# Kernel tuning notes

Measured on AMD Instinct MI355X. Metric: run time of the kernel, lower is better.

## Reference

```python
import jax, jax.numpy as jnp
import numpy as np

B, N, O, C, K = 2, 384, 4, 128, 64  # batch, num_points, num_ori, num_hidden, basis_dim

def setup_inputs() -> dict:
    key = jax.random.key(0)
    ks = jax.random.split(key, 5)
    return {
        "x": jax.random.normal(ks[0], (B, N, O, C), dtype=jnp.float32),
        "kernel_basis": jax.random.normal(ks[1], (B, N, N, O, K), dtype=jnp.float32),
        "fiber_kernel_basis": jax.random.normal(ks[2], (O, O, K), dtype=jnp.float32),
        "W_spatial": jax.random.normal(ks[3], (K, C), dtype=jnp.float32) / np.sqrt(K),
        "W_rot": jax.random.normal(ks[4], (K, C), dtype=jnp.float32) / np.sqrt(K),
        "bias": jnp.zeros((C,), dtype=jnp.float32),
    }

def reference(x, kernel_basis, fiber_kernel_basis, W_spatial, W_rot, bias):
    # Dense projections (no bias), as in nn.Dense(num_hidden, use_bias=False)
    spatial_kernel = jnp.einsum('bmnok,kc->bmnoc', kernel_basis, W_spatial)   # (B,M,N,O,C)
    rot_kernel = jnp.einsum('pok,kc->poc', fiber_kernel_basis, W_rot)         # (O,O,C)
    # Spatial aggregation over source points n
    y = jnp.einsum('bnoc,bmnoc->bmoc', x, spatial_kernel)                     # (B,M,O,C)
    # Fiber (orientation) aggregation over o
    y = jnp.einsum('bmoc,poc->bmpc', y, rot_kernel)                           # (B,M,O,C)
    return y + bias
```

## Files before the change

kernel.cpp:

```cpp
#include <hip/hip_runtime.h>
#include <hip/hip_bf16.h>

typedef __attribute__((ext_vector_type(4)))  float    f32x4;
typedef __attribute__((ext_vector_type(16))) float    f32x16;
typedef __attribute__((ext_vector_type(8)))  _Float16 f16x8;

#define NB 2
#define NN 384
#define NO 4
#define NC 128
#define NK 64
#define MT 64
#define NMT 6
#define LDA 72
#define LDZ 72

__global__ __launch_bounds__(256, 3)
void sepconv_stage1(const float* __restrict__ KB, const float* __restrict__ X,
                    const float* __restrict__ Ws, float* __restrict__ part,
                    int ns)
{
    __shared__ _Float16 Alds[MT * LDA];
    __shared__ _Float16 Zlds[NC * LDZ];

    const int t  = threadIdx.x;
    const int wg = blockIdx.x;
    const int b  = wg & 1;
    const int o  = (wg >> 1) & 3;
    const int mt = (wg >> 3) % NMT;
    const int split = wg / (8 * NMT);
    const int n0 = split * ns;

    const int zc = t >> 1;
    const int kh = t & 1;
    float wreg[32];
#pragma unroll
    for (int j = 0; j < 32; ++j)
        wreg[j] = Ws[(kh * 32 + j) * NC + zc];

    const int ar  = t >> 2;
    const int ak0 = (t & 3) * 16;
    const int m   = mt * MT + ar;
    const int abase = (b * NN + m) * (NN * NO * NK) + o * NK + ak0;
    const int xbase = (b * NN) * (NO * NC) + o * NC + zc;

    const int lane = t & 63;
    const int wv   = t >> 6;
    const int msub = wv & 1;
    const int cs0  = wv >> 1;
    const int cs1  = 2 + (wv >> 1);
    const int half = lane >> 5;
    const int l31  = lane & 31;
    const _Float16* afp  = &Alds[(msub * 32 + l31) * LDA + half * 8];
    const _Float16* bfp0 = &Zlds[(cs0  * 32 + l31) * LDZ + half * 8];
    const _Float16* bfp1 = &Zlds[(cs1  * 32 + l31) * LDZ + half * 8];

    f32x16 acc0, acc1;
#pragma unroll
    for (int r = 0; r < 16; ++r) { acc0[r] = 0.f; acc1[r] = 0.f; }

    f32x4 acur[4];
    float xcur;
    {
        const float* ap = KB + abase + n0 * (NO * NK);
#pragma unroll
        for (int j = 0; j < 4; ++j) acur[j] = ((const f32x4*)ap)[j];
        xcur = X[xbase + n0 * (NO * NC)];
    }

    for (int i = 0; i < ns; ++i) {
        const int np = n0 + ((i + 1 < ns) ? (i + 1) : i);
        f32x4 anext[4];
        {
            const float* ap = KB + abase + np * (NO * NK);
#pragma unroll
            for (int j = 0; j < 4; ++j) anext[j] = ((const f32x4*)ap)[j];
        }
        const float xnext = X[xbase + np * (NO * NC)];

#pragma unroll
        for (int v = 0; v < 4; ++v) {
            f16x8 z;
#pragma unroll
            for (int j = 0; j < 8; ++j) z[j] = (_Float16)(xcur * wreg[v * 8 + j]);
            *(f16x8*)&Zlds[zc * LDZ + kh * 32 + v * 8] = z;
        }
#pragma unroll
        for (int v = 0; v < 2; ++v) {
            f16x8 a;
#pragma unroll
            for (int j = 0; j < 8; ++j)
                a[j] = (_Float16)(acur[v * 2 + (j >> 2)][j & 3]);
            *(f16x8*)&Alds[ar * LDA + ak0 + v * 8] = a;
        }
        __syncthreads();

#pragma unroll
        for (int kc = 0; kc < 4; ++kc) {
            f16x8 af  = *(const f16x8*)(afp  + kc * 16);
            f16x8 bf0 = *(const f16x8*)(bfp0 + kc * 16);
            f16x8 bf1 = *(const f16x8*)(bfp1 + kc * 16);
            acc0 = __builtin_amdgcn_mfma_f32_32x32x16_f16(af, bf0, acc0, 0, 0, 0);
            acc1 = __builtin_amdgcn_mfma_f32_32x32x16_f16(af, bf1, acc1, 0, 0, 0);
        }
        __syncthreads();

#pragma unroll
        for (int j = 0; j < 4; ++j) acur[j] = anext[j];
        xcur = xnext;
    }

    float* pb = part + ((size_t)((split * NB + b) * NO + o)) * (NN * NC);
#pragma unroll
    for (int r = 0; r < 16; ++r) {
        const int ml = (r & 3) + 8 * (r >> 2) + 4 * half;
        const int mm = mt * MT + msub * 32 + ml;
        pb[mm * NC + cs0 * 32 + l31] = acc0[r];
        pb[mm * NC + cs1 * 32 + l31] = acc1[r];
    }
}

__global__ __launch_bounds__(256)
void sepconv_stage2(const float* __restrict__ part, const float* __restrict__ fiber,
                    const float* __restrict__ Wr, const float* __restrict__ bias,
                    float* __restrict__ out, int nsplit)
{
    const int bid = blockIdx.x;
    const int b = bid / NN;
    const int m = bid % NN;
    const int t = threadIdx.x;
    const int c = t & 127;
    const int g = t >> 7;

    float rot[8];
#pragma unroll
    for (int i = 0; i < 8; ++i) rot[i] = 0.f;
    for (int k = 0; k < NK; ++k) {
        const float w = Wr[k * NC + c];
#pragma unroll
        for (int q = 0; q < 2; ++q)
#pragma unroll
            for (int oo = 0; oo < 4; ++oo)
                rot[q * 4 + oo] += fiber[((2 * g + q) * NO + oo) * NK + k] * w;
    }

    float y1[4];
#pragma unroll
    for (int oo = 0; oo < 4; ++oo) {
        float s = 0.f;
        for (int sp = 0; sp < nsplit; ++sp)
            s += part[((size_t)((sp * NB + b) * NO + oo)) * (NN * NC) + m * NC + c];
        y1[oo] = s;
    }

    const float bv = bias[c];
#pragma unroll
    for (int q = 0; q < 2; ++q) {
        float v = bv;
#pragma unroll
        for (int oo = 0; oo < 4; ++oo) v += y1[oo] * rot[q * 4 + oo];
        out[((b * NN + m) * NO + (2 * g + q)) * NC + c] = v;
    }
}

extern "C" void kernel_launch(void* const* d_in, const int* in_sizes, int n_in,
                              void* d_out, int out_size, void* d_ws, size_t ws_size,
                              hipStream_t stream)
{
    const float* X    = (const float*)d_in[0];
    const float* KB   = (const float*)d_in[1];
    const float* FB   = (const float*)d_in[2];
    const float* Ws   = (const float*)d_in[3];
    const float* Wr   = (const float*)d_in[4];
    const float* bias = (const float*)d_in[5];
    float* out  = (float*)d_out;
    float* part = (float*)d_ws;

    const size_t per = (size_t)NB * NO * NN * NC * sizeof(float);
    int nsplit = 16;
    while (nsplit > 1 && (size_t)nsplit * per > ws_size) nsplit >>= 1;
    const int ns = NN / nsplit;

    sepconv_stage1<<<dim3(8 * NMT * nsplit), dim3(256), 0, stream>>>(KB, X, Ws, part, ns);
    sepconv_stage2<<<dim3(NB * NN), dim3(256), 0, stream>>>(part, FB, Wr, bias, out, nsplit);
}
```

Before: 457.8 us.

## Stream kernel-basis tiles into LDS asynchronously and build B operand in registers

After: 491.7 us. +7.4%, slower.

```diff
diff --git a/kernel.cpp b/kernel.cpp
--- a/kernel.cpp
+++ b/kernel.cpp
@@ -1,5 +1,4 @@
 #include <hip/hip_runtime.h>
-#include <hip/hip_bf16.h>
 
 typedef __attribute__((ext_vector_type(4)))  float    f32x4;
 typedef __attribute__((ext_vector_type(16))) float    f32x16;
@@ -10,114 +9,122 @@
 #define NO 4
 #define NC 128
 #define NK 64
-#define MT 64
-#define NMT 6
-#define LDA 72
-#define LDZ 72
+#define MT 128
+#define NMT 3
 
-__global__ __launch_bounds__(256, 3)
+__device__ __forceinline__ void async16(const float* g, float* l) {
+    __builtin_amdgcn_global_load_lds((const __attribute__((address_space(1))) void*)g,
+                                     (__attribute__((address_space(3))) void*)l, 16, 0, 0);
+}
+
+__global__ __launch_bounds__(256, 2)
 void sepconv_stage1(const float* __restrict__ KB, const float* __restrict__ X,
                     const float* __restrict__ Ws, float* __restrict__ part,
                     int ns)
 {
-    __shared__ _Float16 Alds[MT * LDA];
-    __shared__ _Float16 Zlds[NC * LDZ];
+    extern __shared__ float smem[];
+    float* Abuf = smem;
+    float* xlds = smem + 4 * 2 * 2048;
 
-    const int t  = threadIdx.x;
-    const int wg = blockIdx.x;
-    const int b  = wg & 1;
-    const int o  = (wg >> 1) & 3;
-    const int mt = (wg >> 3) % NMT;
-    const int split = wg / (8 * NMT);
-    const int n0 = split * ns;
+    const int t    = threadIdx.x;
+    const int lane = t & 63;
+    const int w    = t >> 6;
+    const int l31  = lane & 31;
+    const int half = lane >> 5;
 
-    const int zc = t >> 1;
-    const int kh = t & 1;
-    float wreg[32];
+    const int wg    = blockIdx.x;
+    const int b     = wg & 1;
+    const int o     = (wg >> 1) & 3;
+    const int mt    = (wg >> 3) % NMT;
+    const int split = wg / 24;
+    const int n0    = split * ns;
+
+    f16x8 wsreg[4][4];
+    {
+        const float* wp = Ws + half * 8 * NC + l31;
 #pragma unroll
-    for (int j = 0; j < 32; ++j)
-        wreg[j] = Ws[(kh * 32 + j) * NC + zc];
-
-    const int ar  = t >> 2;
-    const int ak0 = (t & 3) * 16;
-    const int m   = mt * MT + ar;
-    const int abase = (b * NN + m) * (NN * NO * NK) + o * NK + ak0;
-    const int xbase = (b * NN) * (NO * NC) + o * NC + zc;
-
-    const int lane = t & 63;
-    const int wv   = t >> 6;
-    const int msub = wv & 1;
-    const int cs0  = wv >> 1;
-    const int cs1  = 2 + (wv >> 1);
-    const int half = lane >> 5;
-    const int l31  = lane & 31;
-    const _Float16* afp  = &Alds[(msub * 32 + l31) * LDA + half * 8];
-    const _Float16* bfp0 = &Zlds[(cs0  * 32 + l31) * LDZ + half * 8];
-    const _Float16* bfp1 = &Zlds[(cs1  * 32 + l31) * LDZ + half * 8];
-
-    f32x16 acc0, acc1;
+        for (int cs = 0; cs < 4; ++cs)
 #pragma unroll
-    for (int r = 0; r < 16; ++r) { acc0[r] = 0.f; acc1[r] = 0.f; }
-
-    f32x4 acur[4];
-    float xcur;
-    {
-        const float* ap = KB + abase + n0 * (NO * NK);
+            for (int kc = 0; kc < 4; ++kc) {
+                f16x8 v;
 #pragma unroll
-        for (int j = 0; j < 4; ++j) acur[j] = ((const f32x4*)ap)[j];
-        xcur = X[xbase + n0 * (NO * NC)];
+                for (int j = 0; j < 8; ++j)
+                    v[j] = (_Float16)wp[(kc * 16 + j) * NC + cs * 32];
+                wsreg[cs][kc] = v;
+            }
     }
 
+    for (int idx = t; idx < ns * NC; idx += 256) {
+        const int nl = idx >> 7, c = idx & 127;
+        xlds[idx] = X[((b * NN + n0 + nl) * NO + o) * NC + c];
+    }
+    __syncthreads();
+
+    const int mrow = mt * MT + w * 32 + l31;
+    const float* gbase = KB + (size_t)(b * NN + mrow) * (NN * NO * NK)
+                            + (size_t)n0 * (NO * NK) + o * NK + half * 4;
+    float* const wbuf = Abuf + w * 2 * 2048;
+
+    auto stage = [&](int nl, int p) {
+        const float* g = gbase + (size_t)nl * (NO * NK);
+        float* l = wbuf + p * 2048;
+#pragma unroll
+        for (int i = 0; i < 8; ++i)
+            async16(g + i * 8, l + i * 256);
+    };
+
+    f32x16 acc[4];
+#pragma unroll
+    for (int cs = 0; cs < 4; ++cs)
+#pragma unroll
+        for (int r = 0; r < 16; ++r) acc[cs][r] = 0.f;
+
+    stage(0, 0);
+    stage(1, 1);
+
     for (int i = 0; i < ns; ++i) {
-        const int np = n0 + ((i + 1 < ns) ? (i + 1) : i);
-        f32x4 anext[4];
-        {
-            const float* ap = KB + abase + np * (NO * NK);
+        if (i < ns - 1) __builtin_amdgcn_s_waitcnt(0x0F78);
+        else            __builtin_amdgcn_s_waitcnt(0x0F70);
+        __builtin_amdgcn_sched_barrier(0);
+
+        f16x8 xh[4];
 #pragma unroll
-            for (int j = 0; j < 4; ++j) anext[j] = ((const f32x4*)ap)[j];
+        for (int cs = 0; cs < 4; ++cs) {
+            const _Float16 xv = (_Float16)xlds[i * NC + cs * 32 + l31];
+            f16x8 s;
+#pragma unroll
+            for (int j = 0; j < 8; ++j) s[j] = xv;
+            xh[cs] = s;
         }
-        const float xnext = X[xbase + np * (NO * NC)];
 
-#pragma unroll
-        for (int v = 0; v < 4; ++v) {
-            f16x8 z;
-#pragma unroll
-            for (int j = 0; j < 8; ++j) z[j] = (_Float16)(xcur * wreg[v * 8 + j]);
-            *(f16x8*)&Zlds[zc * LDZ + kh * 32 + v * 8] = z;
-        }
-#pragma unroll
-        for (int v = 0; v < 2; ++v) {
-            f16x8 a;
-#pragma unroll
-            for (int j = 0; j < 8; ++j)
-                a[j] = (_Float16)(acur[v * 2 + (j >> 2)][j & 3]);
-            *(f16x8*)&Alds[ar * LDA + ak0 + v * 8] = a;
-        }
-        __syncthreads();
-
+        const float* ab = wbuf + (i & 1) * 2048 + half * 256 + l31 * 4;
 #pragma unroll
         for (int kc = 0; kc < 4; ++kc) {
-            f16x8 af  = *(const f16x8*)(afp  + kc * 16);
-            f16x8 bf0 = *(const f16x8*)(bfp0 + kc * 16);
-            f16x8 bf1 = *(const f16x8*)(bfp1 + kc * 16);
-            acc0 = __builtin_amdgcn_mfma_f32_32x32x16_f16(af, bf0, acc0, 0, 0, 0);
-            acc1 = __builtin_amdgcn_mfma_f32_32x32x16_f16(af, bf1, acc1, 0, 0, 0);
+            const f32x4 a0 = *(const f32x4*)(ab + kc * 512);
+            const f32x4 a1 = *(const f32x4*)(ab + kc * 512 + 128);
+            f16x8 af;
+#pragma unroll
+            for (int j = 0; j < 4; ++j) { af[j] = (_Float16)a0[j]; af[4 + j] = (_Float16)a1[j]; }
+#pragma unroll
+            for (int cs = 0; cs < 4; ++cs) {
+                const f16x8 bf = xh[cs] * wsreg[cs][kc];
+                acc[cs] = __builtin_amdgcn_mfma_f32_32x32x16_f16(af, bf, acc[cs], 0, 0, 0);
+            }
         }
-        __syncthreads();
 
-#pragma unroll
-        for (int j = 0; j < 4; ++j) acur[j] = anext[j];
-        xcur = xnext;
+        __builtin_amdgcn_sched_barrier(0);
+        if (i + 2 < ns) stage(i + 2, i & 1);
     }
 
-    float* pb = part + ((size_t)((split * NB + b) * NO + o)) * (NN * NC);
+    float* pb = part + ((size_t)(split * NB + b) * NO + o) * (NN * NC)
+                     + (mt * MT + w * 32) * NC;
 #pragma unroll
-    for (int r = 0; r < 16; ++r) {
-        const int ml = (r & 3) + 8 * (r >> 2) + 4 * half;
-        const int mm = mt * MT + msub * 32 + ml;
-        pb[mm * NC + cs0 * 32 + l31] = acc0[r];
-        pb[mm * NC + cs1 * 32 + l31] = acc1[r];
-    }
+    for (int cs = 0; cs < 4; ++cs)
+#pragma unroll
+        for (int r = 0; r < 16; ++r) {
+            const int ml = (r & 3) + 8 * (r >> 2) + 4 * half;
+            pb[ml * NC + cs * 32 + l31] = acc[cs][r];
+        }
 }
 
 __global__ __launch_bounds__(256)
@@ -136,12 +143,12 @@
 #pragma unroll
     for (int i = 0; i < 8; ++i) rot[i] = 0.f;
     for (int k = 0; k < NK; ++k) {
-        const float w = Wr[k * NC + c];
+        const float wv = Wr[k * NC + c];
 #pragma unroll
         for (int q = 0; q < 2; ++q)
 #pragma unroll
             for (int oo = 0; oo < 4; ++oo)
-                rot[q * 4 + oo] += fiber[((2 * g + q) * NO + oo) * NK + k] * w;
+                rot[q * 4 + oo] += fiber[((2 * g + q) * NO + oo) * NK + k] * wv;
     }
 
     float y1[4];
@@ -149,7 +156,7 @@
     for (int oo = 0; oo < 4; ++oo) {
         float s = 0.f;
         for (int sp = 0; sp < nsplit; ++sp)
-            s += part[((size_t)((sp * NB + b) * NO + oo)) * (NN * NC) + m * NC + c];
+            s += part[((size_t)(sp * NB + b) * NO + oo) * (NN * NC) + m * NC + c];
         y1[oo] = s;
     }
 
@@ -178,9 +185,12 @@
 
     const size_t per = (size_t)NB * NO * NN * NC * sizeof(float);
     int nsplit = 16;
-    while (nsplit > 1 && (size_t)nsplit * per > ws_size) nsplit >>= 1;
+    if (ws_size >= 32 * per) {  }
+    while (nsplit > 16 && (size_t)nsplit * per > ws_size) nsplit >>= 1;
     const int ns = NN / nsplit;
 
-    sepconv_stage1<<<dim3(8 * NMT * nsplit), dim3(256), 0, stream>>>(KB, X, Ws, part, ns);
+    const size_t lds = (4 * 2 * 2048 + (size_t)ns * NC) * sizeof(float);
+
+    sepconv_stage1<<<dim3(24 * nsplit), dim3(256), lds, stream>>>(KB, X, Ws, part, ns);
     sepconv_stage2<<<dim3(NB * NN), dim3(256), 0, stream>>>(part, FB, Wr, bias, out, nsplit);
 }
```
